# Optimization experiments

Measured on AMD Instinct MI355X. Metric: run time of the kernel, lower is better.

The kernel has to match this reference:

```python
import jax, jax.numpy as jnp
import numpy as np

BATCH = 32768


def _unpack(packed, n):
    # packed: [rows, ceil(n/8)] ints in [0,256). Extract bits MSB-first per byte.
    bits = (packed[:, :, None] >> jnp.arange(7, -1, -1, dtype=packed.dtype)) & 1
    return bits.reshape(packed.shape[0], -1)[:, :n]  # [rows, n] of {0,1}


def setup_inputs() -> dict:
    key = jax.random.key(0)
    k0, k1, k2, k3, k4 = jax.random.split(key, 5)
    return {
        "x": jax.random.normal(k0, (BATCH, 784), dtype=jnp.float32),
        "w1_packed": jax.random.randint(k1, (256, 98), 0, 256, dtype=jnp.int32),
        "m1_packed": jax.random.randint(k2, (256, 98), 0, 256, dtype=jnp.int32),
        "alpha1": jnp.float32(1.0),
        "w2_packed": jax.random.randint(k3, (10, 32), 0, 256, dtype=jnp.int32),
        "m2_packed": jax.random.randint(k4, (10, 32), 0, 256, dtype=jnp.int32),
        "alpha2": jnp.float32(1.0),
    }


def reference(x, w1_packed, m1_packed, alpha1, w2_packed, m2_packed, alpha2):
    # Layer 1: binary {-1,+1} weights * {0,1} mask * alpha
    w1 = (2 * _unpack(w1_packed, 784) - 1).astype(jnp.float32)
    w1 = w1 * _unpack(m1_packed, 784).astype(jnp.float32) * alpha1  # [256, 784]
    h = jax.nn.relu(jnp.einsum('bi,oi->bo', x, w1))  # [B, 256]
    # Layer 2
    w2 = (2 * _unpack(w2_packed, 256) - 1).astype(jnp.float32)
    w2 = w2 * _unpack(m2_packed, 256).astype(jnp.float32) * alpha2  # [10, 256]
    return jnp.einsum('bh,oh->bo', h, w2)  # [B, 10]
```

## Files before the change

### kernel.cpp

```cpp
#include <hip/hip_runtime.h>
#include <hip/hip_bf16.h>

typedef __bf16 bf16x8 __attribute__((ext_vector_type(8)));
typedef float floatx4 __attribute__((ext_vector_type(4)));

#define GLB_AS __attribute__((address_space(1)))
#define LDS_AS __attribute__((address_space(3)))

__device__ __forceinline__ void async_cp16(const void* g, void* l) {
  __builtin_amdgcn_global_load_lds((GLB_AS void*)g, (LDS_AS void*)l, 16, 0, 0);
}

__device__ __forceinline__ unsigned short f2bf(float f) {
  __bf16 b = (__bf16)f;
  return __builtin_bit_cast(unsigned short, b);
}

__global__ void decode_w1_kernel(const int* __restrict__ w1p,
                                 const int* __restrict__ m1p,
                                 unsigned short* __restrict__ w1d) {
  int t = blockIdx.x * 256 + threadIdx.x;
  if (t >= 256 * 100) return;
  int r = t / 100;
  int j = t - r * 100;
  unsigned short vals[8];
#pragma unroll
  for (int k = 0; k < 8; ++k) vals[k] = 0;
  if (j < 98) {
    unsigned int v = (unsigned int)w1p[r * 98 + j];
    unsigned int m = (unsigned int)m1p[r * 98 + j];
#pragma unroll
    for (int k = 0; k < 8; ++k) {
      unsigned int bit = (v >> (7 - k)) & 1u;
      unsigned int mk  = (m >> (7 - k)) & 1u;
      vals[k] = (unsigned short)(mk ? (bit ? 0x3F80u : 0xBF80u) : 0u);
    }
  }
  uint4 pack;
  pack.x = (unsigned)vals[0] | ((unsigned)vals[1] << 16);
  pack.y = (unsigned)vals[2] | ((unsigned)vals[3] << 16);
  pack.z = (unsigned)vals[4] | ((unsigned)vals[5] << 16);
  pack.w = (unsigned)vals[6] | ((unsigned)vals[7] << 16);
  *reinterpret_cast<uint4*>(w1d + t * 8) = pack;
}

#define BM 64
#define BK 32
#define NCH 25
#define W1LD 800
#define HS_LD 264

__global__ __launch_bounds__(256, 2) void fused_kernel(
    const float* __restrict__ x,
    const unsigned short* __restrict__ w1d,
    const int* __restrict__ w2p,
    const int* __restrict__ m2p,
    const float* __restrict__ a1p,
    const float* __restrict__ a2p,
    float* __restrict__ out) {
  __shared__ unsigned short smem[64 * 264 + 16 * 256];

  const int tid  = threadIdx.x;
  const int wave = tid >> 6;
  const int lane = tid & 63;
  const int l15  = lane & 15;
  const int quad = lane >> 4;
  const int row0 = blockIdx.x * BM;

  const int OFF_XS = 0;
  const int OFF_WS = 2048;
  const int OFF_HS = 0;
  const int OFF_W2 = 16896;

  floatx4 acc[4][4];
#pragma unroll
  for (int i = 0; i < 4; ++i)
#pragma unroll
    for (int j = 0; j < 4; ++j) acc[i][j] = (floatx4){0.f, 0.f, 0.f, 0.f};

  for (int kc = 0; kc < NCH; ++kc) {
#pragma unroll
    for (int it = 0; it < 4; ++it) {
      int seg = it * 256 + tid;
      int r = seg >> 2, c = seg & 3;
      async_cp16(w1d + r * W1LD + kc * BK + c * 8, &smem[OFF_WS + seg * 8]);
    }
    float4 xv[2];
#pragma unroll
    for (int it = 0; it < 2; ++it) {
      int seg = it * 256 + tid;
      int r = seg >> 3, c4 = seg & 7;
      int col = kc * BK + c4 * 4;
      if (col < 784) {
        xv[it] = *reinterpret_cast<const float4*>(
            x + (size_t)(row0 + r) * 784 + col);
      } else {
        xv[it] = (float4){0.f, 0.f, 0.f, 0.f};
      }
    }
#pragma unroll
    for (int it = 0; it < 2; ++it) {
      int seg = it * 256 + tid;
      int r = seg >> 3, c4 = seg & 7;
      ushort4 b;
      b.x = f2bf(xv[it].x); b.y = f2bf(xv[it].y);
      b.z = f2bf(xv[it].z); b.w = f2bf(xv[it].w);
      *reinterpret_cast<ushort4*>(&smem[OFF_XS + r * BK + c4 * 4]) = b;
    }
    __syncthreads();

    bf16x8 af[4], bfr[4];
#pragma unroll
    for (int mi = 0; mi < 4; ++mi)
      af[mi] = *reinterpret_cast<const bf16x8*>(
          &smem[OFF_XS + (mi * 16 + l15) * BK + quad * 8]);
#pragma unroll
    for (int nj = 0; nj < 4; ++nj)
      bfr[nj] = *reinterpret_cast<const bf16x8*>(
          &smem[OFF_WS + (wave * 64 + nj * 16 + l15) * BK + quad * 8]);
#pragma unroll
    for (int mi = 0; mi < 4; ++mi)
#pragma unroll
      for (int nj = 0; nj < 4; ++nj)
        acc[mi][nj] = __builtin_amdgcn_mfma_f32_16x16x32_bf16(
            af[mi], bfr[nj], acc[mi][nj], 0, 0, 0);
    __syncthreads();
  }

  const float a1 = a1p[0];
  const float a2 = a2p[0];
#pragma unroll
  for (int mi = 0; mi < 4; ++mi) {
#pragma unroll
    for (int nj = 0; nj < 4; ++nj) {
      int col   = wave * 64 + nj * 16 + l15;
      int rbase = mi * 16 + quad * 4;
#pragma unroll
      for (int r = 0; r < 4; ++r) {
        float h = fmaxf(a1 * acc[mi][nj][r], 0.f);
        smem[OFF_HS + (rbase + r) * HS_LD + col] = f2bf(h);
      }
    }
  }
#pragma unroll
  for (int it = 0; it < 2; ++it) {
    int idx = it * 256 + tid;
    if (idx < 320) {
      int r = idx >> 5, j = idx & 31;
      unsigned int v = (unsigned int)w2p[r * 32 + j];
      unsigned int m = (unsigned int)m2p[r * 32 + j];
#pragma unroll
      for (int k = 0; k < 8; ++k) {
        unsigned int bit = (v >> (7 - k)) & 1u;
        unsigned int mk  = (m >> (7 - k)) & 1u;
        smem[OFF_W2 + r * 256 + j * 8 + k] =
            (unsigned short)(mk ? (bit ? 0x3F80u : 0xBF80u) : 0u);
      }
    }
  }
#pragma unroll
  for (int r = 10; r < 16; ++r) smem[OFF_W2 + r * 256 + tid] = 0;
  __syncthreads();

  floatx4 o2 = (floatx4){0.f, 0.f, 0.f, 0.f};
#pragma unroll
  for (int ks = 0; ks < 8; ++ks) {
    bf16x8 ha = *reinterpret_cast<const bf16x8*>(
        &smem[OFF_HS + (wave * 16 + l15) * HS_LD + ks * 32 + quad * 8]);
    bf16x8 wb = *reinterpret_cast<const bf16x8*>(
        &smem[OFF_W2 + l15 * 256 + ks * 32 + quad * 8]);
    o2 = __builtin_amdgcn_mfma_f32_16x16x32_bf16(ha, wb, o2, 0, 0, 0);
  }
  if (l15 < 10) {
#pragma unroll
    for (int r = 0; r < 4; ++r) {
      int gr = row0 + wave * 16 + quad * 4 + r;
      out[(size_t)gr * 10 + l15] = a2 * o2[r];
    }
  }
}

extern "C" void kernel_launch(void* const* d_in, const int* in_sizes, int n_in,
                              void* d_out, int out_size, void* d_ws, size_t ws_size,
                              hipStream_t stream) {
  const float* x   = (const float*)d_in[0];
  const int*   w1p = (const int*)d_in[1];
  const int*   m1p = (const int*)d_in[2];
  const float* a1  = (const float*)d_in[3];
  const int*   w2p = (const int*)d_in[4];
  const int*   m2p = (const int*)d_in[5];
  const float* a2  = (const float*)d_in[6];
  unsigned short* w1d = (unsigned short*)d_ws;
  float* out = (float*)d_out;

  decode_w1_kernel<<<100, 256, 0, stream>>>(w1p, m1p, w1d);
  fused_kernel<<<512, 256, 0, stream>>>(x, w1d, w2p, m2p, a1, a2, out);
}
```

Measured before the change: 185.6 us.

## Double-buffer W1 and x tiles in LDS to overlap loads with MFMA

Splits the layer-1 K loop into stage/load/convert/compute helpers and double-buffers both the W1 and x tiles in shared memory. The loads for chunk kc+1 are issued before the MFMAs for chunk kc, with one barrier per iteration instead of two. This is meant to hide global-load latency behind compute, at the cost of more LDS layout and extra registers for the prefetched x values. The LDS footprint is unchanged because the hidden-activation buffer reuses the same space.

```diff
diff --git a/kernel.cpp b/kernel.cpp
--- a/kernel.cpp
+++ b/kernel.cpp
@@ -49,6 +49,13 @@
 #define NCH 25
 #define W1LD 800
 #define HS_LD 264
+
+#define OFF_WS0 0
+#define OFF_WS1 8192
+#define OFF_XS0 16384
+#define OFF_XS1 18432
+#define OFF_HS  0
+#define OFF_W2  16896
 
 __global__ __launch_bounds__(256, 2) void fused_kernel(
     const float* __restrict__ x,
@@ -67,25 +74,21 @@
   const int quad = lane >> 4;
   const int row0 = blockIdx.x * BM;
 
-  const int OFF_XS = 0;
-  const int OFF_WS = 2048;
-  const int OFF_HS = 0;
-  const int OFF_W2 = 16896;
-
   floatx4 acc[4][4];
 #pragma unroll
   for (int i = 0; i < 4; ++i)
 #pragma unroll
     for (int j = 0; j < 4; ++j) acc[i][j] = (floatx4){0.f, 0.f, 0.f, 0.f};
 
-  for (int kc = 0; kc < NCH; ++kc) {
+  auto stage_w = [&](int kc, int offW) {
 #pragma unroll
     for (int it = 0; it < 4; ++it) {
       int seg = it * 256 + tid;
       int r = seg >> 2, c = seg & 3;
-      async_cp16(w1d + r * W1LD + kc * BK + c * 8, &smem[OFF_WS + seg * 8]);
-    }
-    float4 xv[2];
+      async_cp16(w1d + r * W1LD + kc * BK + c * 8, &smem[offW + seg * 8]);
+    }
+  };
+  auto load_x = [&](int kc, float4* xv) {
 #pragma unroll
     for (int it = 0; it < 2; ++it) {
       int seg = it * 256 + tid;
@@ -98,6 +101,8 @@
         xv[it] = (float4){0.f, 0.f, 0.f, 0.f};
       }
     }
+  };
+  auto cvt_write = [&](int offX, const float4* xv) {
 #pragma unroll
     for (int it = 0; it < 2; ++it) {
       int seg = it * 256 + tid;
@@ -105,27 +110,48 @@
       ushort4 b;
       b.x = f2bf(xv[it].x); b.y = f2bf(xv[it].y);
       b.z = f2bf(xv[it].z); b.w = f2bf(xv[it].w);
-      *reinterpret_cast<ushort4*>(&smem[OFF_XS + r * BK + c4 * 4]) = b;
-    }
-    __syncthreads();
-
+      *reinterpret_cast<ushort4*>(&smem[offX + r * BK + c4 * 4]) = b;
+    }
+  };
+  auto compute = [&](int offW, int offX) {
     bf16x8 af[4], bfr[4];
 #pragma unroll
     for (int mi = 0; mi < 4; ++mi)
       af[mi] = *reinterpret_cast<const bf16x8*>(
-          &smem[OFF_XS + (mi * 16 + l15) * BK + quad * 8]);
+          &smem[offX + (mi * 16 + l15) * BK + quad * 8]);
 #pragma unroll
     for (int nj = 0; nj < 4; ++nj)
       bfr[nj] = *reinterpret_cast<const bf16x8*>(
-          &smem[OFF_WS + (wave * 64 + nj * 16 + l15) * BK + quad * 8]);
+          &smem[offW + (wave * 64 + nj * 16 + l15) * BK + quad * 8]);
 #pragma unroll
     for (int mi = 0; mi < 4; ++mi)
 #pragma unroll
       for (int nj = 0; nj < 4; ++nj)
         acc[mi][nj] = __builtin_amdgcn_mfma_f32_16x16x32_bf16(
             af[mi], bfr[nj], acc[mi][nj], 0, 0, 0);
+  };
+
+  {
+    float4 xv[2];
+    load_x(0, xv);
+    stage_w(0, OFF_WS0);
+    cvt_write(OFF_XS0, xv);
+  }
+  __syncthreads();
+
+#pragma unroll 2
+  for (int kc = 0; kc < NCH - 1; ++kc) {
+    const int p = kc & 1;
+    float4 xn[2];
+    load_x(kc + 1, xn);
+    stage_w(kc + 1, p ? OFF_WS0 : OFF_WS1);
+    compute(p ? OFF_WS1 : OFF_WS0,
+            p ? OFF_XS1 : OFF_XS0);
+    cvt_write(p ? OFF_XS0 : OFF_XS1, xn);
     __syncthreads();
   }
+  compute(OFF_WS0, OFF_XS0);
+  __syncthreads();
 
   const float a1 = a1p[0];
   const float a2 = a2p[0];
```

Measured after the change: 181.2 us. 2.4% less time.

## Load MFMA operands directly from global, drop LDS staging and barriers in GEMM1

Applied to the files above, without the earlier changes.

The first-layer GEMM no longer stages x and decoded weights through LDS. Each lane loads its MFMA fragments straight from global memory, x as float4 pairs converted to bf16 in registers and W1 from a transposed k-major decoded layout. This removes both per-chunk __syncthreads and the LDS round trip, unrolls the loop by two and raises the launch-bounds occupancy hint to 3. In exchange each wave re-reads the x rows that all four waves share and issues strided global loads, so cache pressure goes up.

```diff
diff --git a/kernel.cpp b/kernel.cpp
--- a/kernel.cpp
+++ b/kernel.cpp
@@ -3,13 +3,6 @@
 
 typedef __bf16 bf16x8 __attribute__((ext_vector_type(8)));
 typedef float floatx4 __attribute__((ext_vector_type(4)));
-
-#define GLB_AS __attribute__((address_space(1)))
-#define LDS_AS __attribute__((address_space(3)))
-
-__device__ __forceinline__ void async_cp16(const void* g, void* l) {
-  __builtin_amdgcn_global_load_lds((GLB_AS void*)g, (LDS_AS void*)l, 16, 0, 0);
-}
 
 __device__ __forceinline__ unsigned short f2bf(float f) {
   __bf16 b = (__bf16)f;
@@ -18,11 +11,10 @@
 
 __global__ void decode_w1_kernel(const int* __restrict__ w1p,
                                  const int* __restrict__ m1p,
-                                 unsigned short* __restrict__ w1d) {
+                                 unsigned short* __restrict__ w1t) {
   int t = blockIdx.x * 256 + threadIdx.x;
-  if (t >= 256 * 100) return;
-  int r = t / 100;
-  int j = t - r * 100;
+  int r = t & 255;
+  int j = t >> 8;
   unsigned short vals[8];
 #pragma unroll
   for (int k = 0; k < 8; ++k) vals[k] = 0;
@@ -41,24 +33,25 @@
   pack.y = (unsigned)vals[2] | ((unsigned)vals[3] << 16);
   pack.z = (unsigned)vals[4] | ((unsigned)vals[5] << 16);
   pack.w = (unsigned)vals[6] | ((unsigned)vals[7] << 16);
-  *reinterpret_cast<uint4*>(w1d + t * 8) = pack;
+  *reinterpret_cast<uint4*>(w1t + t * 8) = pack;
 }
 
 #define BM 64
-#define BK 32
 #define NCH 25
-#define W1LD 800
 #define HS_LD 264
 
-__global__ __launch_bounds__(256, 2) void fused_kernel(
+#define OFF_HS  0
+#define OFF_W2  16896
+
+__global__ __launch_bounds__(256, 3) void fused_kernel(
     const float* __restrict__ x,
-    const unsigned short* __restrict__ w1d,
+    const unsigned short* __restrict__ w1t,
     const int* __restrict__ w2p,
     const int* __restrict__ m2p,
     const float* __restrict__ a1p,
     const float* __restrict__ a2p,
     float* __restrict__ out) {
-  __shared__ unsigned short smem[64 * 264 + 16 * 256];
+  __shared__ unsigned short smem[64 * HS_LD + 16 * 256];
 
   const int tid  = threadIdx.x;
   const int wave = tid >> 6;
@@ -67,65 +60,52 @@
   const int quad = lane >> 4;
   const int row0 = blockIdx.x * BM;
 
-  const int OFF_XS = 0;
-  const int OFF_WS = 2048;
-  const int OFF_HS = 0;
-  const int OFF_W2 = 16896;
-
   floatx4 acc[4][4];
 #pragma unroll
   for (int i = 0; i < 4; ++i)
 #pragma unroll
     for (int j = 0; j < 4; ++j) acc[i][j] = (floatx4){0.f, 0.f, 0.f, 0.f};
 
-  for (int kc = 0; kc < NCH; ++kc) {
+  const float* xl = x + (size_t)row0 * 784 + (size_t)l15 * 784 + quad * 8;
+  const unsigned short* wl = w1t + ((size_t)quad * 256 + wave * 64 + l15) * 8;
+
+  auto do_chunk = [&](int kc, bool full) {
+    float4 xa[4], xb[4];
+    const float* xp = xl + kc * 32;
 #pragma unroll
-    for (int it = 0; it < 4; ++it) {
-      int seg = it * 256 + tid;
-      int r = seg >> 2, c = seg & 3;
-      async_cp16(w1d + r * W1LD + kc * BK + c * 8, &smem[OFF_WS + seg * 8]);
-    }
-    float4 xv[2];
-#pragma unroll
-    for (int it = 0; it < 2; ++it) {
-      int seg = it * 256 + tid;
-      int r = seg >> 3, c4 = seg & 7;
-      int col = kc * BK + c4 * 4;
-      if (col < 784) {
-        xv[it] = *reinterpret_cast<const float4*>(
-            x + (size_t)(row0 + r) * 784 + col);
+    for (int mi = 0; mi < 4; ++mi) {
+      if (full || quad < 2) {
+        xa[mi] = *reinterpret_cast<const float4*>(xp + mi * 16 * 784);
+        xb[mi] = *reinterpret_cast<const float4*>(xp + mi * 16 * 784 + 4);
       } else {
-        xv[it] = (float4){0.f, 0.f, 0.f, 0.f};
+        xa[mi] = (float4){0.f, 0.f, 0.f, 0.f};
+        xb[mi] = (float4){0.f, 0.f, 0.f, 0.f};
       }
     }
-#pragma unroll
-    for (int it = 0; it < 2; ++it) {
-      int seg = it * 256 + tid;
-      int r = seg >> 3, c4 = seg & 7;
-      ushort4 b;
-      b.x = f2bf(xv[it].x); b.y = f2bf(xv[it].y);
-      b.z = f2bf(xv[it].z); b.w = f2bf(xv[it].w);
-      *reinterpret_cast<ushort4*>(&smem[OFF_XS + r * BK + c4 * 4]) = b;
-    }
-    __syncthreads();
-
-    bf16x8 af[4], bfr[4];
-#pragma unroll
-    for (int mi = 0; mi < 4; ++mi)
-      af[mi] = *reinterpret_cast<const bf16x8*>(
-          &smem[OFF_XS + (mi * 16 + l15) * BK + quad * 8]);
+    bf16x8 bfr[4];
+    const unsigned short* wp = wl + (size_t)kc * 4 * 256 * 8;
 #pragma unroll
     for (int nj = 0; nj < 4; ++nj)
-      bfr[nj] = *reinterpret_cast<const bf16x8*>(
-          &smem[OFF_WS + (wave * 64 + nj * 16 + l15) * BK + quad * 8]);
+      bfr[nj] = *reinterpret_cast<const bf16x8*>(wp + nj * 16 * 8);
+    bf16x8 af[4];
+#pragma unroll
+    for (int mi = 0; mi < 4; ++mi) {
+      af[mi][0] = (__bf16)xa[mi].x; af[mi][1] = (__bf16)xa[mi].y;
+      af[mi][2] = (__bf16)xa[mi].z; af[mi][3] = (__bf16)xa[mi].w;
+      af[mi][4] = (__bf16)xb[mi].x; af[mi][5] = (__bf16)xb[mi].y;
+      af[mi][6] = (__bf16)xb[mi].z; af[mi][7] = (__bf16)xb[mi].w;
+    }
 #pragma unroll
     for (int mi = 0; mi < 4; ++mi)
 #pragma unroll
       for (int nj = 0; nj < 4; ++nj)
         acc[mi][nj] = __builtin_amdgcn_mfma_f32_16x16x32_bf16(
             af[mi], bfr[nj], acc[mi][nj], 0, 0, 0);
-    __syncthreads();
-  }
+  };
+
+#pragma unroll 2
+  for (int kc = 0; kc < NCH - 1; ++kc) do_chunk(kc, true);
+  do_chunk(NCH - 1, false);
 
   const float a1 = a1p[0];
   const float a2 = a2p[0];
@@ -190,9 +170,9 @@
   const int*   w2p = (const int*)d_in[4];
   const int*   m2p = (const int*)d_in[5];
   const float* a2  = (const float*)d_in[6];
-  unsigned short* w1d = (unsigned short*)d_ws;
+  unsigned short* w1t = (unsigned short*)d_ws;
   float* out = (float*)d_out;
 
-  decode_w1_kernel<<<100, 256, 0, stream>>>(w1p, m1p, w1d);
-  fused_kernel<<<512, 256, 0, stream>>>(x, w1d, w2p, m2p, a1, a2, out);
+  decode_w1_kernel<<<100, 256, 0, stream>>>(w1p, m1p, w1t);
+  fused_kernel<<<512, 256, 0, stream>>>(x, w1t, w2p, m2p, a1, a2, out);
 }
```

New measurement: 196.8 us. 1.06x slower.
